# Kernel tuning notes

Hardware: AMD Instinct MI355X
Metric: run time of the kernel (lower is better)

The kernel has to match this reference:

```python
import jax, jax.numpy as jnp
import numpy as np

B, N, CIN, COUT, P = 16, 10000, 8, 32, 8
E = 160000
TRAIN_OR_PREDICT = 1


def setup_inputs() -> dict:
    key = jax.random.key(0)
    ks = jax.random.split(key, 12)
    inp = {}
    inp["X"] = jax.random.normal(ks[0], (B, N, CIN, 2 * P), dtype=jnp.float32)
    inp["edge_index"] = jax.random.randint(ks[1], (2, E), 0, N, dtype=jnp.int64)
    inp["edge_weight"] = jax.random.uniform(ks[2], (E,), dtype=jnp.float32)
    inp["attention"] = jax.random.uniform(ks[3], (2 * P,), dtype=jnp.float32)
    sc = 1.0 / np.sqrt(CIN)
    sl = 1.0 / np.sqrt(2 * COUT)
    names = ["z", "r", "h"]
    for i, g in enumerate(names):
        inp["Wc" + g] = jax.random.normal(ks[4 + i], (CIN, COUT), dtype=jnp.float32) * sc
        inp["bc" + g] = jnp.zeros((COUT,), dtype=jnp.float32)
        inp["Wl" + g] = jax.random.normal(ks[7 + i], (2 * COUT, COUT), dtype=jnp.float32) * sl
        inp["bl" + g] = jnp.zeros((COUT,), dtype=jnp.float32)
    return inp


def _gcn_norm(edge_index, edge_weight, n):
    # PyG gcn_norm: add self-loops (weight 1.0), symmetric D^-1/2 (A+I) D^-1/2
    src, dst = edge_index[0], edge_index[1]
    loop = jnp.arange(n)
    src = jnp.concatenate([src, loop])
    dst = jnp.concatenate([dst, loop])
    w = jnp.concatenate([edge_weight, jnp.ones((n,), edge_weight.dtype)])
    deg = jax.ops.segment_sum(w, dst, num_segments=n)
    dinv = jnp.where(deg > 0, deg ** -0.5, 0.0)
    return src, dst, dinv[src] * w * dinv[dst]


def _gcn(X, W, b, src, dst, norm, n):
    # propagate-then-transform: (A_hat X) W + b  (linear, identical to X W then A_hat)
    msg = X[:, src, :] * norm[None, :, None]                     # (B, E', Cin)
    agg = jax.ops.segment_sum(jnp.swapaxes(msg, 0, 1), dst, num_segments=n)  # (N, B, Cin)
    return jnp.einsum('bni,io->bno', jnp.swapaxes(agg, 0, 1), W) + b


def reference(X, edge_index, edge_weight, attention,
              Wcz, bcz, Wlz, blz, Wcr, bcr, Wlr, blr, Wch, bch, Wlh, blh):
    b_, n, _, t2 = X.shape
    p = t2 // 2
    src, dst, norm = _gcn_norm(edge_index, edge_weight, n)
    probs = jax.nn.softmax(attention)
    # backward half of the sum is scaled by TrainorPredict (linearity of the weighted sum)
    ws = jnp.concatenate([probs[:p], probs[p:] * TRAIN_OR_PREDICT])
    H0 = jnp.zeros((b_, n, Wlz.shape[1]), X.dtype)
    Xs = jnp.moveaxis(X, 3, 0)  # (2P, B, N, Cin); H is never chained in the original loop

    def cell(x):
        Z = jax.nn.sigmoid(jnp.concatenate([_gcn(x, Wcz, bcz, src, dst, norm, n), H0], -1) @ Wlz + blz)
        R = jax.nn.sigmoid(jnp.concatenate([_gcn(x, Wcr, bcr, src, dst, norm, n), H0], -1) @ Wlr + blr)
        Ht = jnp.tanh(jnp.concatenate([_gcn(x, Wch, bch, src, dst, norm, n), H0 * R], -1) @ Wlh + blh)
        return Z * H0 + (1.0 - Z) * Ht

    def step(acc, pw):
        x, w = pw
        return acc + w * cell(x), None

    out, _ = jax.lax.scan(step, H0, (Xs, ws))
    return out
```

## Files before the change

### kernel.cpp

```cpp
#include <hip/hip_runtime.h>
#include <stdint.h>

#define NN 10000
#define NE 160000
#define NB 16
#define NT 4

typedef __attribute__((ext_vector_type(8))) float f32x8;
typedef __attribute__((ext_vector_type(4))) float f32x4;
typedef __attribute__((ext_vector_type(2))) float f32x2;
typedef __attribute__((ext_vector_type(8))) _Float16 h16x8;

#define AGG_LD 136

__device__ __forceinline__ int ei_stride(const int* __restrict__ ei) {
    int z = ei[1] | ei[3] | ei[5] | ei[7] | ei[9] | ei[11] | ei[13] | ei[15];
    return (z == 0) ? 2 : 1;
}

__global__ __launch_bounds__(256)
void k_prep(const float* __restrict__ X, h16x8* __restrict__ X2, int do_repack,
            const int* __restrict__ ei, const float* __restrict__ ew,
            float* deg, int* count,
            const float* __restrict__ attn,
            const float* __restrict__ Wcz, const float* __restrict__ bcz,
            const float* __restrict__ Wlz, const float* __restrict__ blz,
            const float* __restrict__ Wch, const float* __restrict__ bch,
            const float* __restrict__ Wlh, const float* __restrict__ blh,
            float* consts) {
    int gid = blockIdx.x * blockDim.x + threadIdx.x;
    int gsz = gridDim.x * blockDim.x;
    int stride = ei_stride(ei);
    for (int e = gid; e < NE; e += gsz) {
        int d = ei[(size_t)(NE + e) * stride];
        atomicAdd(&deg[d], ew[e]);
        atomicAdd(&count[d], 1);
    }
    if (do_repack) {
        const int total = NN * 256;
        for (int i = gid; i < total; i += gsz) {
            int n = i >> 8, t = i & 255;
            int b = t >> 4, chunk = t & 15;
            f32x8 w = ((const f32x8*)X)[((size_t)b * NN + n) * 16 + chunk];
            h16x8 h;
            #pragma unroll
            for (int j = 0; j < 8; ++j) h[j] = (_Float16)w[j];
            X2[((size_t)(b >> 1) * NN + n) * 32 + (b & 1) * 16 + chunk] = h;
        }
    }
    if (blockIdx.x == 0) {
        int tid = threadIdx.x;
        {
            int c = tid >> 5, o = tid & 31;
            float mz = 0.f, mh = 0.f;
            for (int k = 0; k < 32; ++k) {
                mz += Wcz[c * 32 + k] * Wlz[k * 32 + o];
                mh += Wch[c * 32 + k] * Wlh[k * 32 + o];
            }
            consts[tid] = mz;
            consts[256 + tid] = mh;
        }
        if (tid < 32) {
            float cz = blz[tid], ch = blh[tid];
            for (int k = 0; k < 32; ++k) {
                cz += bcz[k] * Wlz[k * 32 + tid];
                ch += bch[k] * Wlh[k * 32 + tid];
            }
            consts[512 + tid] = cz;
            consts[544 + tid] = ch;
        }
        if (tid == 0) {
            float a[16], m = -1e30f, s = 0.f;
            for (int t = 0; t < 16; ++t) { a[t] = attn[t]; m = fmaxf(m, a[t]); }
            for (int t = 0; t < 16; ++t) { a[t] = __expf(a[t] - m); s += a[t]; }
            for (int t = 0; t < 16; ++t) consts[576 + t] = a[t] / s;
        }
    }
}

__global__ void k_scan(const float* __restrict__ deg, const int* __restrict__ count,
                       float* dinv, int* offsets, int* fillptr) {
    int tid = threadIdx.x;
    int lane = tid & 63, wv = tid >> 6;
    __shared__ int wsum[16];
    __shared__ int carry;
    if (tid == 0) carry = 0;
    __syncthreads();
    for (int base = 0; base < NN; base += 1024) {
        int i = base + tid;
        int v = (i < NN) ? count[i] : 0;
        int x = v;
        #pragma unroll
        for (int s = 1; s < 64; s <<= 1) {
            int y = __shfl_up(x, s, 64);
            if (lane >= s) x += y;
        }
        if (lane == 63) wsum[wv] = x;
        __syncthreads();
        if (wv == 0 && lane < 16) {
            int y = wsum[lane];
            #pragma unroll
            for (int s = 1; s < 16; s <<= 1) {
                int z = __shfl_up(y, s, 64);
                if (lane >= s) y += z;
            }
            wsum[lane] = y;
        }
        __syncthreads();
        int wbase = (wv == 0) ? 0 : wsum[wv - 1];
        int incl = carry + wbase + x;
        int excl = incl - v;
        if (i < NN) { offsets[i] = excl; fillptr[i] = excl; }
        __syncthreads();
        if (tid == 1023) carry = incl;
        __syncthreads();
    }
    for (int i = tid; i < NN; i += 1024) dinv[i] = rsqrtf(deg[i] + 1.0f);
}

__global__ void k_fill(const int* __restrict__ ei, const float* __restrict__ ew,
                       const float* __restrict__ dinv,
                       int* fillptr, int* csr_sn) {
    int e = blockIdx.x * blockDim.x + threadIdx.x;
    if (e >= NE) return;
    int stride = ei_stride(ei);
    int s = ei[(size_t)e * stride];
    int d = ei[(size_t)(NE + e) * stride];
    int pos = atomicAdd(&fillptr[d], 1);
    csr_sn[2 * pos]     = s * 32;
    csr_sn[2 * pos + 1] = __float_as_int(dinv[s] * ew[e] * dinv[d]);
}

__device__ __forceinline__ float gatefn(float uz, float uh) {
    float ez = __expf(uz);
    float eh = __expf(2.f * uh);
    return (eh - 1.f) * __builtin_amdgcn_rcpf((1.f + ez) * (eh + 1.f));
}

__global__ __launch_bounds__(256)
void k_main_h(const h16x8* __restrict__ X2,
              const int* __restrict__ offsets, const int* __restrict__ count,
              const float* __restrict__ dinv,
              const int* __restrict__ csr_sn,
              const float* __restrict__ consts,
              float* __restrict__ out) {
    __shared__ float sAgg[2 * NT * AGG_LD];
    __shared__ float sMz[256], sMh[256], sCz[32], sCh[32], sWs[16];
    int tid = threadIdx.x;
    int bp   = blockIdx.x & 7;
    int tile = blockIdx.x >> 3;

    sMz[tid] = consts[tid];
    sMh[tid] = consts[256 + tid];
    if (tid < 32) { sCz[tid] = consts[512 + tid]; sCh[tid] = consts[544 + tid]; }
    if (tid < 16) sWs[tid] = consts[576 + tid];

    int lane = tid & 63;
    int wv = __builtin_amdgcn_readfirstlane(tid >> 6);
    int half = lane >> 5;
    int chunk = lane & 31;
    int n = tile * NT + wv;
    const h16x8* xb = X2 + ((size_t)bp * NN) * 32;
    float dn = dinv[n];
    float selfn = (half == 0) ? dn * dn : 0.f;
    float acc[8];
    {
        h16x8 w = xb[(size_t)n * 32 + chunk];
        #pragma unroll
        for (int j = 0; j < 8; ++j) acc[j] = selfn * (float)w[j];
    }
    int off = __builtin_amdgcn_readfirstlane(offsets[n]);
    int cnt = __builtin_amdgcn_readfirstlane(count[n]);
    const int* snp = csr_sn + 2 * off;
    int e = 0;
    if (cnt >= 8) {
        int p[16], q[16], r[16];
        #pragma unroll
        for (int k = 0; k < 16; ++k) p[k] = snp[k];
        h16x8 A0 = xb[(size_t)(half ? p[2]  : p[0])  + chunk];
        h16x8 A1 = xb[(size_t)(half ? p[6]  : p[4])  + chunk];
        h16x8 A2 = xb[(size_t)(half ? p[10] : p[8])  + chunk];
        h16x8 A3 = xb[(size_t)(half ? p[14] : p[12]) + chunk];
        #pragma unroll
        for (int k = 0; k < 16; ++k) q[k] = snp[16 + k];
        for (e = 8; e + 8 <= cnt; e += 8) {
            h16x8 B0 = xb[(size_t)(half ? q[2]  : q[0])  + chunk];
            h16x8 B1 = xb[(size_t)(half ? q[6]  : q[4])  + chunk];
            h16x8 B2 = xb[(size_t)(half ? q[10] : q[8])  + chunk];
            h16x8 B3 = xb[(size_t)(half ? q[14] : q[12]) + chunk];
            #pragma unroll
            for (int k = 0; k < 16; ++k) r[k] = snp[2 * e + 16 + k];
            float na0 = __int_as_float(half ? p[3]  : p[1]);
            float na1 = __int_as_float(half ? p[7]  : p[5]);
            float na2 = __int_as_float(half ? p[11] : p[9]);
            float na3 = __int_as_float(half ? p[15] : p[13]);
            __builtin_amdgcn_sched_barrier(0);
            #pragma unroll
            for (int j = 0; j < 8; ++j) acc[j] += na0 * (float)A0[j];
            #pragma unroll
            for (int j = 0; j < 8; ++j) acc[j] += na1 * (float)A1[j];
            #pragma unroll
            for (int j = 0; j < 8; ++j) acc[j] += na2 * (float)A2[j];
            #pragma unroll
            for (int j = 0; j < 8; ++j) acc[j] += na3 * (float)A3[j];
            A0 = B0; A1 = B1; A2 = B2; A3 = B3;
            #pragma unroll
            for (int k = 0; k < 16; ++k) { p[k] = q[k]; q[k] = r[k]; }
        }
        {
            float na0 = __int_as_float(half ? p[3]  : p[1]);
            float na1 = __int_as_float(half ? p[7]  : p[5]);
            float na2 = __int_as_float(half ? p[11] : p[9]);
            float na3 = __int_as_float(half ? p[15] : p[13]);
            #pragma unroll
            for (int j = 0; j < 8; ++j) acc[j] += na0 * (float)A0[j];
            #pragma unroll
            for (int j = 0; j < 8; ++j) acc[j] += na1 * (float)A1[j];
            #pragma unroll
            for (int j = 0; j < 8; ++j) acc[j] += na2 * (float)A2[j];
            #pragma unroll
            for (int j = 0; j < 8; ++j) acc[j] += na3 * (float)A3[j];
        }
    }
    for (; e + 2 <= cnt; e += 2) {
        int sa   = half ? snp[2 * e + 2] : snp[2 * e];
        float na = __int_as_float(half ? snp[2 * e + 3] : snp[2 * e + 1]);
        h16x8 w = xb[(size_t)sa + chunk];
        #pragma unroll
        for (int j = 0; j < 8; ++j) acc[j] += na * (float)w[j];
    }
    if (e < cnt) {
        int sa = snp[2 * e];
        float na = half ? 0.f : __int_as_float(snp[2 * e + 1]);
        h16x8 w = xb[(size_t)sa + chunk];
        #pragma unroll
        for (int j = 0; j < 8; ++j) acc[j] += na * (float)w[j];
    }
    #pragma unroll
    for (int j = 0; j < 8; ++j) acc[j] += __shfl_xor(acc[j], 32);
    if (lane < 32) {
        int bl = chunk >> 4;
        int sub = chunk & 15;
        int rr = wv * 2 + bl;
        int c = sub >> 1;
        int tpb = (sub & 1) * 4;
        float* rowp = &sAgg[rr * AGG_LD + c * 2];
        #pragma unroll
        for (int k = 0; k < 4; ++k) {
            f32x2 v = {acc[2 * k], acc[2 * k + 1]};
            *(f32x2*)&rowp[(tpb + k) * 16] = v;
        }
    }
    __syncthreads();

    int o = tid & 31, rr = tid >> 5;
    float mz[8], mh[8];
    #pragma unroll
    for (int c = 0; c < 8; ++c) { mz[c] = sMz[c * 32 + o]; mh[c] = sMh[c * 32 + o]; }
    float czo = sCz[o], cho = sCh[o];
    const f32x4* r0 = (const f32x4*)&sAgg[rr * AGG_LD];
    f32x2 o0 = {0.f, 0.f};
    #pragma unroll
    for (int tp = 0; tp < 8; ++tp) {
        f32x4 A0[4];
        #pragma unroll
        for (int k = 0; k < 4; ++k) A0[k] = r0[tp * 4 + k];
        f32x2 uz = {czo, czo}, uh = {cho, cho};
        #pragma unroll
        for (int k = 0; k < 4; ++k) {
            f32x2 pv = A0[k].xy, qv = A0[k].zw;
            uz += pv * mz[2 * k]; uz += qv * mz[2 * k + 1];
            uh += pv * mh[2 * k]; uh += qv * mh[2 * k + 1];
        }
        f32x2 wsp = {sWs[2 * tp], sWs[2 * tp + 1]};
        f32x2 g;
        g.x = gatefn(uz.x, uh.x);
        g.y = gatefn(uz.y, uh.y);
        o0 += wsp * g;
    }
    int b  = bp * 2 + (rr & 1);
    int n2 = tile * NT + (rr >> 1);
    out[((size_t)b * NN + n2) * 32 + o] = o0.x + o0.y;
}

__global__ __launch_bounds__(256)
void k_main_f32(const float* __restrict__ X,
                const int* __restrict__ offsets, const int* __restrict__ count,
                const float* __restrict__ dinv,
                const int* __restrict__ csr_sn,
                const float* __restrict__ consts,
                float* __restrict__ out) {
    __shared__ float sAgg[NB * 128];
    __shared__ float sMz[256], sMh[256], sCz[32], sCh[32], sWs[16];
    int tid = threadIdx.x;
    int n = blockIdx.x;

    sMz[tid] = consts[tid];
    sMh[tid] = consts[256 + tid];
    if (tid < 32) { sCz[tid] = consts[512 + tid]; sCh[tid] = consts[544 + tid]; }
    if (tid < 16) sWs[tid] = consts[576 + tid];

    int b = tid >> 4, chunk = tid & 15;
    const f32x8* xv = (const f32x8*)X;
    float dn = dinv[n];
    float selfn = dn * dn;
    float acc[8];
    {
        f32x8 w = xv[((size_t)b * NN + n) * 16 + chunk];
        #pragma unroll
        for (int j = 0; j < 8; ++j) acc[j] = selfn * w[j];
    }
    int off = offsets[n], cnt = count[n];
    for (int e = off; e < off + cnt; ++e) {
        int s32 = csr_sn[2 * e];
        float nrm = __int_as_float(csr_sn[2 * e + 1]);
        f32x8 w = xv[(size_t)b * NN * 16 + (size_t)(s32 >> 1) + chunk];
        #pragma unroll
        for (int j = 0; j < 8; ++j) acc[j] += nrm * w[j];
    }
    #pragma unroll
    for (int j = 0; j < 8; ++j) sAgg[tid * 8 + j] = acc[j];
    __syncthreads();

    int o = tid & 31, b0 = tid >> 5;
    float mz[8], mh[8];
    #pragma unroll
    for (int c = 0; c < 8; ++c) { mz[c] = sMz[c * 32 + o]; mh[c] = sMh[c * 32 + o]; }
    float czo = sCz[o], cho = sCh[o];
    float acc0 = 0.f, acc1 = 0.f;
    #pragma unroll
    for (int t = 0; t < 16; ++t) {
        float uz0 = czo, uh0 = cho, uz1 = czo, uh1 = cho;
        #pragma unroll
        for (int c = 0; c < 8; ++c) {
            float a0 = sAgg[b0 * 128 + c * 16 + t];
            float a1 = sAgg[(b0 + 8) * 128 + c * 16 + t];
            uz0 += a0 * mz[c]; uh0 += a0 * mh[c];
            uz1 += a1 * mz[c]; uh1 += a1 * mh[c];
        }
        float w = sWs[t];
        acc0 += w * gatefn(uz0, uh0);
        acc1 += w * gatefn(uz1, uh1);
    }
    out[((size_t)b0 * NN + n) * 32 + o]       = acc0;
    out[((size_t)(b0 + 8) * NN + n) * 32 + o] = acc1;
}

extern "C" void kernel_launch(void* const* d_in, const int* in_sizes, int n_in,
                              void* d_out, int out_size, void* d_ws, size_t ws_size,
                              hipStream_t stream) {
    const float* X    = (const float*)d_in[0];
    const int*   ei   = (const int*)d_in[1];
    const float* ew   = (const float*)d_in[2];
    const float* attn = (const float*)d_in[3];
    const float* Wcz  = (const float*)d_in[4];
    const float* bcz  = (const float*)d_in[5];
    const float* Wlz  = (const float*)d_in[6];
    const float* blz  = (const float*)d_in[7];
    const float* Wch  = (const float*)d_in[12];
    const float* bch  = (const float*)d_in[13];
    const float* Wlh  = (const float*)d_in[14];
    const float* blh  = (const float*)d_in[15];
    float* out = (float*)d_out;

    const size_t x2_bytes = (size_t)NN * 256 * 16;
    const size_t small_bytes = (size_t)NN * 4 * 5 + (size_t)NE * 8 + 592 * 4;
    bool use_h = (ws_size >= x2_bytes + small_bytes);

    char* p = (char*)d_ws;
    h16x8* X2 = nullptr;
    if (use_h) { X2 = (h16x8*)p; p += x2_bytes; }
    float* deg      = (float*)p; p += NN * 4;
    int*   count    = (int*)p;   p += NN * 4;
    float* dinv     = (float*)p; p += NN * 4;
    int*   offsets  = (int*)p;   p += NN * 4;
    int*   fillptr  = (int*)p;   p += NN * 4;
    int*   csr_sn   = (int*)p;   p += (size_t)NE * 8;
    float* consts   = (float*)p; p += 592 * 4;

    hipMemsetAsync(deg, 0, (size_t)NN * 8, stream);
    hipLaunchKernelGGL(k_prep, dim3(1280), dim3(256), 0, stream,
                       X, X2, use_h ? 1 : 0, ei, ew, deg, count,
                       attn, Wcz, bcz, Wlz, blz, Wch, bch, Wlh, blh, consts);
    hipLaunchKernelGGL(k_scan, dim3(1), dim3(1024), 0, stream,
                       deg, count, dinv, offsets, fillptr);
    hipLaunchKernelGGL(k_fill, dim3((NE + 255) / 256), dim3(256), 0, stream,
                       ei, ew, dinv, fillptr, csr_sn);
    if (use_h) {
        hipLaunchKernelGGL(k_main_h, dim3((NN / NT) * 8), dim3(256), 0, stream,
                           X2, offsets, count, dinv, csr_sn, consts, out);
    } else {
        hipLaunchKernelGGL(k_main_f32, dim3(NN), dim3(256), 0, stream,
                           X, offsets, count, dinv, csr_sn, consts, out);
    }
}
```

Measured before the change: 155.1 us.

## Pad CSR rows to multiples of eight and process one batch per block

Each CSR row is padded to a multiple of 8 with zero-weight entries, and the CSR buffer is zeroed by a memset, so the main gather loop runs on whole groups with no tail code. The fp16 copy of X is now a straight elementwise conversion in batch-major layout, and each block handles one batch instead of a pair, which doubles the grid. Within a wave, four edge lanes split the work and are combined with shuffles. The costs are an extra memset, more padded edge reads, and half the lanes sitting idle in the output stage.

```diff
diff --git a/kernel.cpp b/kernel.cpp
--- a/kernel.cpp
+++ b/kernel.cpp
@@ -5,11 +5,13 @@
 #define NE 160000
 #define NB 16
 #define NT 4
+#define CSR_CAP (NE + 8 * NN)
 
 typedef __attribute__((ext_vector_type(8))) float f32x8;
 typedef __attribute__((ext_vector_type(4))) float f32x4;
 typedef __attribute__((ext_vector_type(2))) float f32x2;
 typedef __attribute__((ext_vector_type(8))) _Float16 h16x8;
+typedef __attribute__((ext_vector_type(2))) int i32x2;
 
 #define AGG_LD 136
 
@@ -19,7 +21,7 @@
 }
 
 __global__ __launch_bounds__(256)
-void k_prep(const float* __restrict__ X, h16x8* __restrict__ X2, int do_repack,
+void k_prep(const float* __restrict__ X, h16x8* __restrict__ X3, int do_repack,
             const int* __restrict__ ei, const float* __restrict__ ew,
             float* deg, int* count,
             const float* __restrict__ attn,
@@ -37,15 +39,13 @@
         atomicAdd(&count[d], 1);
     }
     if (do_repack) {
-        const int total = NN * 256;
+        const int total = NN * 16 * NB;
         for (int i = gid; i < total; i += gsz) {
-            int n = i >> 8, t = i & 255;
-            int b = t >> 4, chunk = t & 15;
-            f32x8 w = ((const f32x8*)X)[((size_t)b * NN + n) * 16 + chunk];
+            f32x8 w = ((const f32x8*)X)[i];
             h16x8 h;
             #pragma unroll
             for (int j = 0; j < 8; ++j) h[j] = (_Float16)w[j];
-            X2[((size_t)(b >> 1) * NN + n) * 32 + (b & 1) * 16 + chunk] = h;
+            X3[i] = h;
         }
     }
     if (blockIdx.x == 0) {
@@ -88,7 +88,7 @@
     __syncthreads();
     for (int base = 0; base < NN; base += 1024) {
         int i = base + tid;
-        int v = (i < NN) ? count[i] : 0;
+        int v = (i < NN) ? ((count[i] + 7) & ~7) : 0;
         int x = v;
         #pragma unroll
         for (int s = 1; s < 64; s <<= 1) {
@@ -127,7 +127,7 @@
     int s = ei[(size_t)e * stride];
     int d = ei[(size_t)(NE + e) * stride];
     int pos = atomicAdd(&fillptr[d], 1);
-    csr_sn[2 * pos]     = s * 32;
+    csr_sn[2 * pos]     = s * 16;
     csr_sn[2 * pos + 1] = __float_as_int(dinv[s] * ew[e] * dinv[d]);
 }
 
@@ -138,17 +138,20 @@
 }
 
 __global__ __launch_bounds__(256)
-void k_main_h(const h16x8* __restrict__ X2,
+void k_main_h(const h16x8* __restrict__ X3,
               const int* __restrict__ offsets, const int* __restrict__ count,
               const float* __restrict__ dinv,
               const int* __restrict__ csr_sn,
               const float* __restrict__ consts,
               float* __restrict__ out) {
-    __shared__ float sAgg[2 * NT * AGG_LD];
+    __shared__ float sAgg[NT * AGG_LD];
     __shared__ float sMz[256], sMh[256], sCz[32], sCh[32], sWs[16];
     int tid = threadIdx.x;
-    int bp   = blockIdx.x & 7;
-    int tile = blockIdx.x >> 3;
+    const int G2 = (NN / NT) * 8;
+    int hf = (blockIdx.x >= G2) ? 1 : 0;
+    int local = blockIdx.x - hf * G2;
+    int b = (local & 7) + 8 * hf;
+    int tile = local >> 3;
 
     sMz[tid] = consts[tid];
     sMh[tid] = consts[256 + tid];
@@ -157,94 +160,61 @@
 
     int lane = tid & 63;
     int wv = __builtin_amdgcn_readfirstlane(tid >> 6);
-    int half = lane >> 5;
-    int chunk = lane & 31;
+    int eq = lane >> 4;
+    int chunk = lane & 15;
     int n = tile * NT + wv;
-    const h16x8* xb = X2 + ((size_t)bp * NN) * 32;
+    const h16x8* xb = X3 + (size_t)b * NN * 16;
     float dn = dinv[n];
-    float selfn = (half == 0) ? dn * dn : 0.f;
+    float selfn = (eq == 0) ? dn * dn : 0.f;
     float acc[8];
     {
-        h16x8 w = xb[(size_t)n * 32 + chunk];
+        h16x8 w = xb[(size_t)n * 16 + chunk];
         #pragma unroll
         for (int j = 0; j < 8; ++j) acc[j] = selfn * (float)w[j];
     }
     int off = __builtin_amdgcn_readfirstlane(offsets[n]);
     int cnt = __builtin_amdgcn_readfirstlane(count[n]);
-    const int* snp = csr_sn + 2 * off;
-    int e = 0;
-    if (cnt >= 8) {
-        int p[16], q[16], r[16];
-        #pragma unroll
-        for (int k = 0; k < 16; ++k) p[k] = snp[k];
-        h16x8 A0 = xb[(size_t)(half ? p[2]  : p[0])  + chunk];
-        h16x8 A1 = xb[(size_t)(half ? p[6]  : p[4])  + chunk];
-        h16x8 A2 = xb[(size_t)(half ? p[10] : p[8])  + chunk];
-        h16x8 A3 = xb[(size_t)(half ? p[14] : p[12]) + chunk];
-        #pragma unroll
-        for (int k = 0; k < 16; ++k) q[k] = snp[16 + k];
-        for (e = 8; e + 8 <= cnt; e += 8) {
-            h16x8 B0 = xb[(size_t)(half ? q[2]  : q[0])  + chunk];
-            h16x8 B1 = xb[(size_t)(half ? q[6]  : q[4])  + chunk];
-            h16x8 B2 = xb[(size_t)(half ? q[10] : q[8])  + chunk];
-            h16x8 B3 = xb[(size_t)(half ? q[14] : q[12]) + chunk];
-            #pragma unroll
-            for (int k = 0; k < 16; ++k) r[k] = snp[2 * e + 16 + k];
-            float na0 = __int_as_float(half ? p[3]  : p[1]);
-            float na1 = __int_as_float(half ? p[7]  : p[5]);
-            float na2 = __int_as_float(half ? p[11] : p[9]);
-            float na3 = __int_as_float(half ? p[15] : p[13]);
+    int groups = ((cnt + 7) & ~7) >> 3;
+    const i32x2* cb = (const i32x2*)csr_sn + off;
+
+    if (groups >= 1) {
+        i32x2 c0 = cb[eq], c1 = cb[4 + eq];
+        i32x2 d0 = cb[8 + eq], d1 = cb[12 + eq];
+        h16x8 a0 = xb[(size_t)c0.x + chunk];
+        h16x8 a1 = xb[(size_t)c1.x + chunk];
+        for (int g = 1; g < groups; ++g) {
+            i32x2 e0 = cb[(g + 1) * 8 + eq];
+            i32x2 e1 = cb[(g + 1) * 8 + 4 + eq];
+            h16x8 b0 = xb[(size_t)d0.x + chunk];
+            h16x8 b1 = xb[(size_t)d1.x + chunk];
             __builtin_amdgcn_sched_barrier(0);
-            #pragma unroll
-            for (int j = 0; j < 8; ++j) acc[j] += na0 * (float)A0[j];
-            #pragma unroll
-            for (int j = 0; j < 8; ++j) acc[j] += na1 * (float)A1[j];
-            #pragma unroll
-            for (int j = 0; j < 8; ++j) acc[j] += na2 * (float)A2[j];
-            #pragma unroll
-            for (int j = 0; j < 8; ++j) acc[j] += na3 * (float)A3[j];
-            A0 = B0; A1 = B1; A2 = B2; A3 = B3;
-            #pragma unroll
-            for (int k = 0; k < 16; ++k) { p[k] = q[k]; q[k] = r[k]; }
+            float na0 = __int_as_float(c0.y);
+            float na1 = __int_as_float(c1.y);
+            #pragma unroll
+            for (int j = 0; j < 8; ++j) acc[j] += na0 * (float)a0[j];
+            #pragma unroll
+            for (int j = 0; j < 8; ++j) acc[j] += na1 * (float)a1[j];
+            a0 = b0; a1 = b1;
+            c0 = d0; c1 = d1;
+            d0 = e0; d1 = e1;
         }
         {
-            float na0 = __int_as_float(half ? p[3]  : p[1]);
-            float na1 = __int_as_float(half ? p[7]  : p[5]);
-            float na2 = __int_as_float(half ? p[11] : p[9]);
-            float na3 = __int_as_float(half ? p[15] : p[13]);
-            #pragma unroll
-            for (int j = 0; j < 8; ++j) acc[j] += na0 * (float)A0[j];
-            #pragma unroll
-            for (int j = 0; j < 8; ++j) acc[j] += na1 * (float)A1[j];
-            #pragma unroll
-            for (int j = 0; j < 8; ++j) acc[j] += na2 * (float)A2[j];
-            #pragma unroll
-            for (int j = 0; j < 8; ++j) acc[j] += na3 * (float)A3[j];
-        }
-    }
-    for (; e + 2 <= cnt; e += 2) {
-        int sa   = half ? snp[2 * e + 2] : snp[2 * e];
-        float na = __int_as_float(half ? snp[2 * e + 3] : snp[2 * e + 1]);
-        h16x8 w = xb[(size_t)sa + chunk];
-        #pragma unroll
-        for (int j = 0; j < 8; ++j) acc[j] += na * (float)w[j];
-    }
-    if (e < cnt) {
-        int sa = snp[2 * e];
-        float na = half ? 0.f : __int_as_float(snp[2 * e + 1]);
-        h16x8 w = xb[(size_t)sa + chunk];
-        #pragma unroll
-        for (int j = 0; j < 8; ++j) acc[j] += na * (float)w[j];
-    }
+            float na0 = __int_as_float(c0.y);
+            float na1 = __int_as_float(c1.y);
+            #pragma unroll
+            for (int j = 0; j < 8; ++j) acc[j] += na0 * (float)a0[j];
+            #pragma unroll
+            for (int j = 0; j < 8; ++j) acc[j] += na1 * (float)a1[j];
+        }
+    }
+    #pragma unroll
+    for (int j = 0; j < 8; ++j) acc[j] += __shfl_xor(acc[j], 16);
     #pragma unroll
     for (int j = 0; j < 8; ++j) acc[j] += __shfl_xor(acc[j], 32);
-    if (lane < 32) {
-        int bl = chunk >> 4;
-        int sub = chunk & 15;
-        int rr = wv * 2 + bl;
-        int c = sub >> 1;
-        int tpb = (sub & 1) * 4;
-        float* rowp = &sAgg[rr * AGG_LD + c * 2];
+    if (lane < 16) {
+        int c = chunk >> 1;
+        int tpb = (chunk & 1) * 4;
+        float* rowp = &sAgg[wv * AGG_LD + c * 2];
         #pragma unroll
         for (int k = 0; k < 4; ++k) {
             f32x2 v = {acc[2 * k], acc[2 * k + 1]};
@@ -253,15 +223,16 @@
     }
     __syncthreads();
 
-    int o = tid & 31, rr = tid >> 5;
+    int o = lane & 31, hh = lane >> 5;
     float mz[8], mh[8];
     #pragma unroll
     for (int c = 0; c < 8; ++c) { mz[c] = sMz[c * 32 + o]; mh[c] = sMh[c * 32 + o]; }
     float czo = sCz[o], cho = sCh[o];
-    const f32x4* r0 = (const f32x4*)&sAgg[rr * AGG_LD];
+    const f32x4* r0 = (const f32x4*)&sAgg[wv * AGG_LD];
     f32x2 o0 = {0.f, 0.f};
     #pragma unroll
-    for (int tp = 0; tp < 8; ++tp) {
+    for (int tq = 0; tq < 4; ++tq) {
+        int tp = hh * 4 + tq;
         f32x4 A0[4];
         #pragma unroll
         for (int k = 0; k < 4; ++k) A0[k] = r0[tp * 4 + k];
@@ -278,9 +249,9 @@
         g.y = gatefn(uz.y, uh.y);
         o0 += wsp * g;
     }
-    int b  = bp * 2 + (rr & 1);
-    int n2 = tile * NT + (rr >> 1);
-    out[((size_t)b * NN + n2) * 32 + o] = o0.x + o0.y;
+    float partial = o0.x + o0.y;
+    partial += __shfl_xor(partial, 32);
+    if (hh == 0) out[((size_t)b * NN + n) * 32 + o] = partial;
 }
 
 __global__ __launch_bounds__(256)
@@ -312,9 +283,9 @@
     }
     int off = offsets[n], cnt = count[n];
     for (int e = off; e < off + cnt; ++e) {
-        int s32 = csr_sn[2 * e];
+        int s16 = csr_sn[2 * e];
         float nrm = __int_as_float(csr_sn[2 * e + 1]);
-        f32x8 w = xv[(size_t)b * NN * 16 + (size_t)(s32 >> 1) + chunk];
+        f32x8 w = xv[(size_t)b * NN * 16 + (size_t)s16 + chunk];
         #pragma unroll
         for (int j = 0; j < 8; ++j) acc[j] += nrm * w[j];
     }
@@ -363,32 +334,33 @@
     const float* blh  = (const float*)d_in[15];
     float* out = (float*)d_out;
 
-    const size_t x2_bytes = (size_t)NN * 256 * 16;
-    const size_t small_bytes = (size_t)NN * 4 * 5 + (size_t)NE * 8 + 592 * 4;
-    bool use_h = (ws_size >= x2_bytes + small_bytes);
+    const size_t x3_bytes = (size_t)NN * 256 * 16;
+    const size_t small_bytes = (size_t)NN * 4 * 5 + (size_t)CSR_CAP * 8 + 4096;
+    bool use_h = (ws_size >= x3_bytes + small_bytes);
 
     char* p = (char*)d_ws;
-    h16x8* X2 = nullptr;
-    if (use_h) { X2 = (h16x8*)p; p += x2_bytes; }
+    h16x8* X3 = nullptr;
+    if (use_h) { X3 = (h16x8*)p; p += x3_bytes; }
     float* deg      = (float*)p; p += NN * 4;
     int*   count    = (int*)p;   p += NN * 4;
     float* dinv     = (float*)p; p += NN * 4;
     int*   offsets  = (int*)p;   p += NN * 4;
     int*   fillptr  = (int*)p;   p += NN * 4;
-    int*   csr_sn   = (int*)p;   p += (size_t)NE * 8;
+    int*   csr_sn   = (int*)p;   p += (size_t)CSR_CAP * 8;
     float* consts   = (float*)p; p += 592 * 4;
 
     hipMemsetAsync(deg, 0, (size_t)NN * 8, stream);
+    hipMemsetAsync(csr_sn, 0, (size_t)CSR_CAP * 8, stream);
     hipLaunchKernelGGL(k_prep, dim3(1280), dim3(256), 0, stream,
-                       X, X2, use_h ? 1 : 0, ei, ew, deg, count,
+                       X, X3, use_h ? 1 : 0, ei, ew, deg, count,
                        attn, Wcz, bcz, Wlz, blz, Wch, bch, Wlh, blh, consts);
     hipLaunchKernelGGL(k_scan, dim3(1), dim3(1024), 0, stream,
                        deg, count, dinv, offsets, fillptr);
     hipLaunchKernelGGL(k_fill, dim3((NE + 255) / 256), dim3(256), 0, stream,
                        ei, ew, dinv, fillptr, csr_sn);
     if (use_h) {
-        hipLaunchKernelGGL(k_main_h, dim3((NN / NT) * 8), dim3(256), 0, stream,
-                           X2, offsets, count, dinv, csr_sn, consts, out);
+        hipLaunchKernelGGL(k_main_h, dim3((NN / NT) * 16), dim3(256), 0, stream,
+                           X3, offsets, count, dinv, csr_sn, consts, out);
     } else {
         hipLaunchKernelGGL(k_main_f32, dim3(NN), dim3(256), 0, stream,
                            X, offsets, count, dinv, csr_sn, consts, out);
```

Result: slower. 174.6 us (+12.6%).
